# Optimization experiments

Measured on AMD Instinct MI355X. Metric: run time of the kernel, lower is better.

The kernel has to match this reference:

```python
import jax, jax.numpy as jnp
import numpy as np

B, D, L = 16384, 1024, 4


def setup_inputs() -> dict:
    key = jax.random.key(0)
    ks = jax.random.split(key, 5)
    scale = 1.0 / np.sqrt(D)
    x = jax.random.normal(ks[0], (B, D), dtype=jnp.float32)
    # torch nn.Linear default init: U(-1/sqrt(fan_in), 1/sqrt(fan_in))
    Ws = jax.random.uniform(ks[1], (L, D, D), jnp.float32, -scale, scale)
    bs = jax.random.uniform(ks[2], (L, D), jnp.float32, -scale, scale)
    Wo = jax.random.uniform(ks[3], (D, D), jnp.float32, -scale, scale)
    bo = jax.random.uniform(ks[4], (D,), jnp.float32, -scale, scale)
    return {"x": x, "Ws": Ws, "bs": bs, "Wo": Wo, "bo": bo}


def reference(x, Ws, bs, Wo, bo):
    # torch: matmul(x[:, :, None], x[:, None, :]).sum(2) == x * x.sum(-1, keepdims=True)
    interactions = jax.nn.relu(x * jnp.sum(x, axis=-1, keepdims=True))  # (B, D)
    h = x
    for i in range(L):  # fixed small layer count
        h = jax.nn.relu(h @ Ws[i].T + bs[i])  # torch Linear: y = x W^T + b
    out = ((h + interactions) * 0.5) @ Wo.T + bo
    return out
```

## Files before the change

kernel.cpp:

```cpp
#include <hip/hip_runtime.h>


#define DDIM 1024
#define BROWS 16384
#define NIT 8

typedef __attribute__((ext_vector_type(8))) short s8v;
typedef __attribute__((ext_vector_type(4))) float f4v;

__device__ __forceinline__ unsigned short f2bf(float f) {
    unsigned int u = __float_as_uint(f);
    u += 0x7fffu + ((u >> 16) & 1u);
    return (unsigned short)(u >> 16);
}
__device__ __forceinline__ float bf2f(unsigned short u) {
    return __uint_as_float(((unsigned int)u) << 16);
}
__device__ __forceinline__ void gld16(const void* g, void* l) {
    __builtin_amdgcn_global_load_lds(
        (const __attribute__((address_space(1))) unsigned int*)g,
        (__attribute__((address_space(3))) unsigned int*)l, 16, 0, 0);
}
__device__ __forceinline__ void gld16c(const void* g, void* l) {
    __builtin_amdgcn_global_load_lds(
        (const __attribute__((address_space(1))) unsigned int*)g,
        (__attribute__((address_space(3))) unsigned int*)l, 16, 0, 1);
}

__global__ __launch_bounds__(256) void prep_cvt_kernel(
    const float* __restrict__ x,  const float* __restrict__ Ws,
    const float* __restrict__ Wo, unsigned short* __restrict__ xb,
    unsigned short* __restrict__ wb, float* __restrict__ rowsum)
{
    const int t = threadIdx.x;
    if (blockIdx.x < BROWS) {
        const int row = blockIdx.x;
        const float4 v = *(const float4*)(x + (size_t)row * DDIM + t * 4);
        ushort4 o;
        o.x = f2bf(v.x); o.y = f2bf(v.y); o.z = f2bf(v.z); o.w = f2bf(v.w);
        *(ushort4*)(xb + (size_t)row * DDIM + t * 4) = o;
        float s = v.x + v.y + v.z + v.w;
        #pragma unroll
        for (int off = 32; off > 0; off >>= 1) s += __shfl_down(s, off, 64);
        __shared__ float red[4];
        const int wave = t >> 6, lane = t & 63;
        if (lane == 0) red[wave] = s;
        __syncthreads();
        if (t == 0) rowsum[row] = red[0] + red[1] + red[2] + red[3];
    } else {
        const int base = (blockIdx.x - BROWS) * 1024;
        #pragma unroll
        for (int j = 0; j < 4; ++j) {
            const int idx = base + j * 256 + t;
            const float4 v = (idx < 4 * 262144) ? ((const float4*)Ws)[idx]
                                                : ((const float4*)Wo)[idx - 4 * 262144];
            ushort4 o;
            o.x = f2bf(v.x); o.y = f2bf(v.y); o.z = f2bf(v.z); o.w = f2bf(v.w);
            ((ushort4*)wb)[idx] = o;
        }
    }
}

#define MF(a, b, c) __builtin_amdgcn_mfma_f32_16x16x32_bf16(a, b, c, 0, 0, 0)
#define BAR()   __builtin_amdgcn_s_barrier()
#define VMC(n)  asm volatile("s_waitcnt vmcnt(" #n ")" ::: "memory")

#define SWOFF(lr, cc) ((lr) * 128 + ((((cc) ^ ((lr) & 7))) << 4))

#define SHA(src, dst) {                                              \
    gld16c((src) + soff,                   (char*)(dst) + t * 16);   \
    gld16c((src) + soff + (size_t)64 * K,  (char*)(dst) + t * 16 + 8192); }
#define SHB(src, dst) {                                              \
    gld16((src) + soff,                   (char*)(dst) + t * 16);    \
    gld16((src) + soff + (size_t)64 * K,  (char*)(dst) + t * 16 + 8192); }

#define READ_A(P, m0) {                                                               \
    af[0][0] = *(const s8v*)((const char*)(P) + SWOFF((m0) * 16 + mrow,      quad));      \
    af[0][1] = *(const s8v*)((const char*)(P) + SWOFF((m0) * 16 + mrow,      4 + quad));  \
    af[1][0] = *(const s8v*)((const char*)(P) + SWOFF((m0) * 16 + 16 + mrow, quad));      \
    af[1][1] = *(const s8v*)((const char*)(P) + SWOFF((m0) * 16 + 16 + mrow, 4 + quad)); }

#define READ_B(P) {                                                                   \
    bfr[0][0] = *(const s8v*)((const char*)(P) + SWOFF(bl + mrow,      quad));            \
    bfr[0][1] = *(const s8v*)((const char*)(P) + SWOFF(bl + mrow,      4 + quad));        \
    bfr[1][0] = *(const s8v*)((const char*)(P) + SWOFF(bl + 16 + mrow, quad));            \
    bfr[1][1] = *(const s8v*)((const char*)(P) + SWOFF(bl + 16 + mrow, 4 + quad));        \
    bfr[2][0] = *(const s8v*)((const char*)(P) + SWOFF(bl + 32 + mrow, quad));            \
    bfr[2][1] = *(const s8v*)((const char*)(P) + SWOFF(bl + 32 + mrow, 4 + quad));        \
    bfr[3][0] = *(const s8v*)((const char*)(P) + SWOFF(bl + 48 + mrow, quad));            \
    bfr[3][1] = *(const s8v*)((const char*)(P) + SWOFF(bl + 48 + mrow, 4 + quad)); }

#define MMA8(m0, s) {                                              \
    acc[m0][0]       = MF(af[0][s], bfr[0][s], acc[m0][0]);        \
    acc[m0][1]       = MF(af[0][s], bfr[1][s], acc[m0][1]);        \
    acc[m0][2]       = MF(af[0][s], bfr[2][s], acc[m0][2]);        \
    acc[m0][3]       = MF(af[0][s], bfr[3][s], acc[m0][3]);        \
    acc[(m0) + 1][0] = MF(af[1][s], bfr[0][s], acc[(m0) + 1][0]);  \
    acc[(m0) + 1][1] = MF(af[1][s], bfr[1][s], acc[(m0) + 1][1]);  \
    acc[(m0) + 1][2] = MF(af[1][s], bfr[2][s], acc[(m0) + 1][2]);  \
    acc[(m0) + 1][3] = MF(af[1][s], bfr[3][s], acc[(m0) + 1][3]); }

#define MMA16(m0) { __builtin_amdgcn_s_setprio(1); MMA8(m0, 0) MMA8(m0, 1) \
                    __builtin_amdgcn_s_setprio(0); }

__device__ __forceinline__ void xcd_bar(int* bar, int xcd, int ph) {
    __syncthreads();
    if (threadIdx.x == 0) {
        int* c = bar + xcd * 5 + ph;
        atomicAdd(c, 1);
        int guard = 0;
        while (__hip_atomic_load(c, __ATOMIC_RELAXED, __HIP_MEMORY_SCOPE_AGENT) < 32
               && ++guard < (1 << 22))
            __builtin_amdgcn_s_sleep(2);
    }
    __syncthreads();
}

__global__ __launch_bounds__(512, 2) void deepfm_mega(
    const float* __restrict__ bs, const float* __restrict__ bo,
    float* __restrict__ out,
    const unsigned short* __restrict__ xb, unsigned short* __restrict__ h0,
    unsigned short* __restrict__ h1, const unsigned short* __restrict__ wb,
    const float* __restrict__ rsm, int* __restrict__ cnt)
{
    constexpr int K = DDIM, N = DDIM;
    __shared__ unsigned short smem[2][2][2][128 * 64];
    __shared__ int s_T;

    const int t = threadIdx.x;
    const int lane = t & 63;
    const int wid  = t >> 6;
    const int wr   = wid >> 2;
    const int wc   = wid & 3;
    const int mrow = lane & 15;
    const int quad = lane >> 4;

    if (t == 0) {
        unsigned xcc;
        asm volatile("s_getreg_b32 %0, hwreg(HW_REG_XCC_ID)" : "=s"(xcc));
        const int xcd_ = (int)(xcc & 7);
        const int slot = atomicAdd(&cnt[xcd_], 1);
        s_T = xcd_ * 32 + slot;
    }
    __syncthreads();
    const int T = s_T;
    const int xcd = T >> 5;
    const int rowBase = (T >> 2) * 256;
    const int colBase = (T & 3) * 256;
    int* const bar = cnt + 8;

    const int srow = t >> 3;
    const size_t soff = (size_t)srow * K + (size_t)(((t & 7) ^ (srow & 7)) * 8);

    unsigned short* const a00 = &smem[0][0][0][0];
    unsigned short* const a01 = &smem[0][0][1][0];
    unsigned short* const a10 = &smem[0][1][0][0];
    unsigned short* const a11 = &smem[0][1][1][0];
    unsigned short* const b00 = &smem[1][0][0][0];
    unsigned short* const b01 = &smem[1][0][1][0];
    unsigned short* const b10 = &smem[1][1][0][0];
    unsigned short* const b11 = &smem[1][1][1][0];

    const unsigned short* const aR0 = wr ? a01 : a00;
    const unsigned short* const aR1 = wr ? a11 : a10;
    const unsigned short* const bR0 = (wc >> 1) ? b01 : b00;
    const unsigned short* const bR1 = (wc >> 1) ? b11 : b10;
    const int bl = (wc & 1) * 64;

    #pragma unroll 1
    for (int l = 0; l < 5; ++l) {
        const unsigned short* Acur = (l == 0) ? xb : ((l & 1) ? h0 : h1);
        const unsigned short* Bwc  = wb + (size_t)l * DDIM * DDIM;
        const float* bias = (l == 4) ? bo : (bs + (size_t)l * DDIM);
        unsigned short* outb = (l & 1) ? h1 : h0;

        const unsigned short* const Ab0 = Acur + (size_t)rowBase * K;
        const unsigned short* const Ab1 = Ab0 + (size_t)128 * K;
        const unsigned short* const Bb0 = Bwc + (size_t)colBase * K;
        const unsigned short* const Bb1 = Bb0 + (size_t)128 * K;

        f4v acc[8][4] = {};
        s8v af[2][2], bfr[4][2];

        SHA(Ab0,      a00); SHA(Ab1,      a01);
        SHB(Bb0,      b00); SHB(Bb1,      b01);
        SHB(Bb0 + 64, b10); SHB(Bb1 + 64, b11);
        VMC(4);
        BAR();
        READ_B(bR0); READ_A(aR0, 0);

        #pragma unroll 1
        for (int it = 0; it < NIT; ++it) {
            const int ka = it * 128, kb = ka + 64;
            const bool more = it < NIT - 1;

            SHA(Ab0 + kb, a10);
            BAR(); MMA16(0); BAR();
            READ_A(aR0, 2);
            SHA(Ab1 + kb, a11);
            BAR(); MMA16(2); BAR();
            READ_A(aR0, 4);
            if (more) SHB(Bb0 + ka + 128, b00);
            BAR(); MMA16(4); BAR();
            READ_A(aR0, 6);
            if (more) SHB(Bb1 + ka + 128, b01);
            if (more) { VMC(4); } else { VMC(0); }
            BAR();
            MMA16(6);
            READ_B(bR1); READ_A(aR1, 0);
            BAR();

            if (more) SHA(Ab0 + ka + 128, a00);
            BAR(); MMA16(0); BAR();
            READ_A(aR1, 2);
            if (more) SHA(Ab1 + ka + 128, a01);
            BAR(); MMA16(2); BAR();
            READ_A(aR1, 4);
            if (more) SHB(Bb0 + kb + 128, b10);
            BAR(); MMA16(4); BAR();
            READ_A(aR1, 6);
            if (more) SHB(Bb1 + kb + 128, b11);
            if (more) { VMC(4); }
            BAR();
            MMA16(6);
            if (more) { READ_B(bR0); READ_A(aR0, 0); }
            BAR();
        }

        if (l == 4) {
            float* sCf = (float*)smem;
            #pragma unroll 1
            for (int half = 0; half < 2; ++half) {
                __syncthreads();
                if (wr == half) {
                    #pragma unroll
                    for (int ni = 0; ni < 4; ++ni) {
                        const int n = wc * 64 + ni * 16 + mrow;
                        const float bv = bias[colBase + n];
                        #pragma unroll
                        for (int mi = 0; mi < 8; ++mi)
                            #pragma unroll
                            for (int r = 0; r < 4; ++r)
                                sCf[(mi * 16 + quad * 4 + r) * 256 + n] = acc[mi][ni][r] + bv;
                    }
                }
                __syncthreads();
                #pragma unroll
                for (int p = 0; p < 16; ++p) {
                    const int idx = t + p * 512;
                    const int row = idx >> 6, ch = idx & 63;
                    const float4 v = ((const float4*)sCf)[idx];
                    *(float4*)(out + (size_t)(rowBase + half * 128 + row) * N + colBase + ch * 4) = v;
                }
            }
        } else {
            __syncthreads();
            unsigned short* sC = (unsigned short*)smem;
            #pragma unroll
            for (int ni = 0; ni < 4; ++ni) {
                const int n = wc * 64 + ni * 16 + mrow;
                const float bv = bias[colBase + n];
                #pragma unroll
                for (int mi = 0; mi < 8; ++mi)
                    #pragma unroll
                    for (int r = 0; r < 4; ++r) {
                        const int row = wr * 128 + mi * 16 + quad * 4 + r;
                        float v = acc[mi][ni][r] + bv;
                        v = v > 0.f ? v : 0.f;
                        sC[row * 256 + n] = f2bf(v);
                    }
            }
            __syncthreads();
            #pragma unroll
            for (int p = 0; p < 16; ++p) {
                const int idx = t + p * 512;
                const int row = idx >> 5, ch = idx & 31;
                s8v c = *(const s8v*)&sC[row * 256 + ch * 8];
                if (l == 3) {
                    const float rsv = rsm[rowBase + row];
                    const s8v xv = *(const s8v*)&xb[(size_t)(rowBase + row) * DDIM + colBase + ch * 8];
                    #pragma unroll
                    for (int j = 0; j < 8; ++j) {
                        float itv = bf2f((unsigned short)xv[j]) * rsv;
                        itv = itv > 0.f ? itv : 0.f;
                        c[j] = (short)f2bf(0.5f * (bf2f((unsigned short)c[j]) + itv));
                    }
                }
                *(s8v*)&outb[(size_t)(rowBase + row) * DDIM + colBase + ch * 8] = c;
            }
        }

        if (l < 4) xcd_bar(bar, xcd, l);
    }
}

extern "C" void kernel_launch(void* const* d_in, const int* in_sizes, int n_in,
                              void* d_out, int out_size, void* d_ws, size_t ws_size,
                              hipStream_t stream) {
    const float* x  = (const float*)d_in[0];
    const float* Ws = (const float*)d_in[1];
    const float* bs = (const float*)d_in[2];
    const float* Wo = (const float*)d_in[3];
    const float* bo = (const float*)d_in[4];
    float* out = (float*)d_out;

    char* ws = (char*)d_ws;
    unsigned short* xb  = (unsigned short*)(ws);
    unsigned short* h0  = (unsigned short*)(ws + 33554432);
    unsigned short* h1  = (unsigned short*)(ws + 67108864);
    unsigned short* wb  = (unsigned short*)(ws + 100663296);
    float*          rsm = (float*)(ws + 111149056);

    int* cnt = (ws_size >= 111214592 + 256)
                   ? (int*)(ws + 111214592)
                   : (int*)((char*)d_out + 67108864 - 256);

    hipMemsetAsync(cnt, 0, 192, stream);
    prep_cvt_kernel<<<BROWS + 1280, 256, 0, stream>>>(x, Ws, Wo, xb, wb, rsm);
    deepfm_mega<<<dim3(256), dim3(512), 0, stream>>>(bs, bo, out, xb, h0, h1,
                                                     wb, rsm, cnt);
}
```

Before: 382.3 us.

## Split persistent GEMM chain into three launches and fold counter reset into prep

The single persistent kernel that ran all five GEMM layers with per-XCD spin barriers is replaced by a templated kernel launched three times: layers 0-1, layers 2-3, and the output layer alone. The output launch uses blockIdx directly and skips the XCD slot atomics, and the counter memset is folded into the prep kernel so one runtime call disappears. The A-tile loads drop their cache-policy bit and now use the same load as the B tiles. This trades some inter-layer spin barriers for kernel launch boundaries, which costs launch gaps and loses cross-layer residency.

```diff
diff --git a/kernel.cpp b/kernel.cpp
--- a/kernel.cpp
+++ b/kernel.cpp
@@ -21,16 +21,12 @@
         (const __attribute__((address_space(1))) unsigned int*)g,
         (__attribute__((address_space(3))) unsigned int*)l, 16, 0, 0);
 }
-__device__ __forceinline__ void gld16c(const void* g, void* l) {
-    __builtin_amdgcn_global_load_lds(
-        (const __attribute__((address_space(1))) unsigned int*)g,
-        (__attribute__((address_space(3))) unsigned int*)l, 16, 0, 1);
-}
 
 __global__ __launch_bounds__(256) void prep_cvt_kernel(
     const float* __restrict__ x,  const float* __restrict__ Ws,
     const float* __restrict__ Wo, unsigned short* __restrict__ xb,
-    unsigned short* __restrict__ wb, float* __restrict__ rowsum)
+    unsigned short* __restrict__ wb, float* __restrict__ rowsum,
+    int* __restrict__ cnt)
 {
     const int t = threadIdx.x;
     if (blockIdx.x < BROWS) {
@@ -48,6 +44,7 @@
         __syncthreads();
         if (t == 0) rowsum[row] = red[0] + red[1] + red[2] + red[3];
     } else {
+        if (blockIdx.x == BROWS && t < 128) cnt[t] = 0;
         const int base = (blockIdx.x - BROWS) * 1024;
         #pragma unroll
         for (int j = 0; j < 4; ++j) {
@@ -67,11 +64,8 @@
 
 #define SWOFF(lr, cc) ((lr) * 128 + ((((cc) ^ ((lr) & 7))) << 4))
 
-#define SHA(src, dst) {                                              \
-    gld16c((src) + soff,                   (char*)(dst) + t * 16);   \
-    gld16c((src) + soff + (size_t)64 * K,  (char*)(dst) + t * 16 + 8192); }
-#define SHB(src, dst) {                                              \
-    gld16((src) + soff,                   (char*)(dst) + t * 16);    \
+#define SH(src, dst) {                                              \
+    gld16((src) + soff,                   (char*)(dst) + t * 16);   \
     gld16((src) + soff + (size_t)64 * K,  (char*)(dst) + t * 16 + 8192); }
 
 #define READ_A(P, m0) {                                                               \
@@ -106,7 +100,7 @@
 __device__ __forceinline__ void xcd_bar(int* bar, int xcd, int ph) {
     __syncthreads();
     if (threadIdx.x == 0) {
-        int* c = bar + xcd * 5 + ph;
+        int* c = bar + xcd * 4 + ph;
         atomicAdd(c, 1);
         int guard = 0;
         while (__hip_atomic_load(c, __ATOMIC_RELAXED, __HIP_MEMORY_SCOPE_AGENT) < 32
@@ -116,7 +110,8 @@
     __syncthreads();
 }
 
-__global__ __launch_bounds__(512, 2) void deepfm_mega(
+template <int L0, int NL>
+__global__ __launch_bounds__(512, 2) void gemm_chain(
     const float* __restrict__ bs, const float* __restrict__ bo,
     float* __restrict__ out,
     const unsigned short* __restrict__ xb, unsigned short* __restrict__ h0,
@@ -125,7 +120,6 @@
 {
     constexpr int K = DDIM, N = DDIM;
     __shared__ unsigned short smem[2][2][2][128 * 64];
-    __shared__ int s_T;
 
     const int t = threadIdx.x;
     const int lane = t & 63;
@@ -135,15 +129,21 @@
     const int mrow = lane & 15;
     const int quad = lane >> 4;
 
-    if (t == 0) {
-        unsigned xcc;
-        asm volatile("s_getreg_b32 %0, hwreg(HW_REG_XCC_ID)" : "=s"(xcc));
-        const int xcd_ = (int)(xcc & 7);
-        const int slot = atomicAdd(&cnt[xcd_], 1);
-        s_T = xcd_ * 32 + slot;
+    int T;
+    if (NL > 1) {
+        __shared__ int s_T;
+        if (t == 0) {
+            unsigned xcc;
+            asm volatile("s_getreg_b32 %0, hwreg(HW_REG_XCC_ID)" : "=s"(xcc));
+            const int xcd_ = (int)(xcc & 7);
+            const int slot = atomicAdd(&cnt[xcd_], 1);
+            s_T = xcd_ * 32 + slot;
+        }
+        __syncthreads();
+        T = s_T;
+    } else {
+        T = blockIdx.x;
     }
-    __syncthreads();
-    const int T = s_T;
     const int xcd = T >> 5;
     const int rowBase = (T >> 2) * 256;
     const int colBase = (T & 3) * 256;
@@ -167,8 +167,9 @@
     const unsigned short* const bR1 = (wc >> 1) ? b11 : b10;
     const int bl = (wc & 1) * 64;
 
-    #pragma unroll 1
-    for (int l = 0; l < 5; ++l) {
+    #pragma unroll
+    for (int i = 0; i < NL; ++i) {
+        const int l = L0 + i;
         const unsigned short* Acur = (l == 0) ? xb : ((l & 1) ? h0 : h1);
         const unsigned short* Bwc  = wb + (size_t)l * DDIM * DDIM;
         const float* bias = (l == 4) ? bo : (bs + (size_t)l * DDIM);
@@ -182,9 +183,9 @@
         f4v acc[8][4] = {};
         s8v af[2][2], bfr[4][2];
 
-        SHA(Ab0,      a00); SHA(Ab1,      a01);
-        SHB(Bb0,      b00); SHB(Bb1,      b01);
-        SHB(Bb0 + 64, b10); SHB(Bb1 + 64, b11);
+        SH(Ab0,      a00); SH(Ab1,      a01);
+        SH(Bb0,      b00); SH(Bb1,      b01);
+        SH(Bb0 + 64, b10); SH(Bb1 + 64, b11);
         VMC(4);
         BAR();
         READ_B(bR0); READ_A(aR0, 0);
@@ -194,32 +195,32 @@
             const int ka = it * 128, kb = ka + 64;
             const bool more = it < NIT - 1;
 
-            SHA(Ab0 + kb, a10);
+            SH(Ab0 + kb, a10);
             BAR(); MMA16(0); BAR();
             READ_A(aR0, 2);
-            SHA(Ab1 + kb, a11);
+            SH(Ab1 + kb, a11);
             BAR(); MMA16(2); BAR();
             READ_A(aR0, 4);
-            if (more) SHB(Bb0 + ka + 128, b00);
+            if (more) SH(Bb0 + ka + 128, b00);
             BAR(); MMA16(4); BAR();
             READ_A(aR0, 6);
-            if (more) SHB(Bb1 + ka + 128, b01);
+            if (more) SH(Bb1 + ka + 128, b01);
             if (more) { VMC(4); } else { VMC(0); }
             BAR();
             MMA16(6);
             READ_B(bR1); READ_A(aR1, 0);
             BAR();
 
-            if (more) SHA(Ab0 + ka + 128, a00);
+            if (more) SH(Ab0 + ka + 128, a00);
             BAR(); MMA16(0); BAR();
             READ_A(aR1, 2);
-            if (more) SHA(Ab1 + ka + 128, a01);
+            if (more) SH(Ab1 + ka + 128, a01);
             BAR(); MMA16(2); BAR();
             READ_A(aR1, 4);
-            if (more) SHB(Bb0 + kb + 128, b10);
+            if (more) SH(Bb0 + kb + 128, b10);
             BAR(); MMA16(4); BAR();
             READ_A(aR1, 6);
-            if (more) SHB(Bb1 + kb + 128, b11);
+            if (more) SH(Bb1 + kb + 128, b11);
             if (more) { VMC(4); }
             BAR();
             MMA16(6);
@@ -290,7 +291,7 @@
             }
         }
 
-        if (l < 4) xcd_bar(bar, xcd, l);
+        if (NL > 1 && i < NL - 1) xcd_bar(bar, xcd, i);
     }
 }
 
@@ -311,12 +312,12 @@
     unsigned short* wb  = (unsigned short*)(ws + 100663296);
     float*          rsm = (float*)(ws + 111149056);
 
-    int* cnt = (ws_size >= 111214592 + 256)
+    int* cnt = (ws_size >= 111214592 + 512)
                    ? (int*)(ws + 111214592)
-                   : (int*)((char*)d_out + 67108864 - 256);
-
-    hipMemsetAsync(cnt, 0, 192, stream);
-    prep_cvt_kernel<<<BROWS + 1280, 256, 0, stream>>>(x, Ws, Wo, xb, wb, rsm);
-    deepfm_mega<<<dim3(256), dim3(512), 0, stream>>>(bs, bo, out, xb, h0, h1,
-                                                     wb, rsm, cnt);
-}
+                   : (int*)((char*)d_out + 67108864 - 512);
+
+    prep_cvt_kernel<<<BROWS + 1280, 256, 0, stream>>>(x, Ws, Wo, xb, wb, rsm, cnt);
+    gemm_chain<0, 2><<<256, 512, 0, stream>>>(bs, bo, out, xb, h0, h1, wb, rsm, cnt);
+    gemm_chain<2, 2><<<256, 512, 0, stream>>>(bs, bo, out, xb, h0, h1, wb, rsm, cnt + 64);
+    gemm_chain<4, 1><<<256, 512, 0, stream>>>(bs, bo, out, xb, h0, h1, wb, rsm, cnt);
+}
```

After: 332.6 us. -13.0%, faster.
